# Optimization experiments

Hardware: AMD Instinct MI355X
Metric: run time of the kernel (lower is better)

## Reference

```python
import jax, jax.numpy as jnp
import numpy as np

N = 50000   # nodes
E = 640000  # edges
IN, H, OUT = 128, 128, 64
BN_EPS = 1e-5


def setup_inputs() -> dict:
    key = jax.random.key(0)
    ks = jax.random.split(key, 16)
    inp = {}
    inp["x"] = jax.random.normal(ks[0], (N, IN), jnp.float32)
    inp["edge_index"] = jax.random.randint(ks[1], (2, E), 0, N, dtype=jnp.int32)
    # BatchNorm affine params (nontrivial so grads are informative)
    inp["bn_in_gamma"] = 1.0 + 0.1 * jax.random.normal(ks[2], (IN,), jnp.float32)
    inp["bn_in_beta"] = 0.1 * jax.random.normal(ks[3], (IN,), jnp.float32)
    inp["bn1_gamma"] = 1.0 + 0.1 * jax.random.normal(ks[4], (H,), jnp.float32)
    inp["bn1_beta"] = 0.1 * jax.random.normal(ks[5], (H,), jnp.float32)
    inp["bn2_gamma"] = 1.0 + 0.1 * jax.random.normal(ks[6], (OUT,), jnp.float32)
    inp["bn2_beta"] = 0.1 * jax.random.normal(ks[7], (OUT,), jnp.float32)
    # Linear / GCNConv weights (fan-in scaled)
    inp["proj_W"] = jax.random.normal(ks[8], (IN, H), jnp.float32) / np.sqrt(IN)
    inp["proj_b"] = jnp.zeros((H,), jnp.float32)
    inp["conv1_W"] = jax.random.normal(ks[9], (H, H), jnp.float32) / np.sqrt(H)
    inp["conv1_b"] = jnp.zeros((H,), jnp.float32)
    inp["conv2_W"] = jax.random.normal(ks[10], (H, OUT), jnp.float32) / np.sqrt(H)
    inp["conv2_b"] = jnp.zeros((OUT,), jnp.float32)
    return inp


def batchnorm(x, gamma, beta):
    # training-mode BN: batch statistics (biased variance), per-feature affine
    m = jnp.mean(x, axis=0)
    v = jnp.mean(jnp.square(x - m), axis=0)
    return (x - m) * jax.lax.rsqrt(v + BN_EPS) * gamma + beta


def gcn_conv(x, src, dst, W, b):
    # PyG GCNConv: y = D^{-1/2} (A + I) D^{-1/2} (x W) + b
    xw = x @ W                                    # [N, F_out]
    loops = jnp.arange(N, dtype=src.dtype)
    s = jnp.concatenate([src, loops])             # [E + N]
    d = jnp.concatenate([dst, loops])
    deg = jax.ops.segment_sum(jnp.ones_like(d, jnp.float32), d, num_segments=N)
    dinv = jnp.where(deg > 0, jax.lax.rsqrt(deg), 0.0)
    norm = dinv[s] * dinv[d]                      # [E + N]
    msgs = xw[s] * norm[:, None]                  # gather + per-edge scale
    out = jax.ops.segment_sum(msgs, d, num_segments=N)  # scatter-add
    return out + b


def reference(x, edge_index, bn_in_gamma, bn_in_beta, bn1_gamma, bn1_beta,
              bn2_gamma, bn2_beta, proj_W, proj_b, conv1_W, conv1_b,
              conv2_W, conv2_b):
    src, dst = edge_index[0], edge_index[1]
    h = batchnorm(x, bn_in_gamma, bn_in_beta)
    h = jax.nn.relu(h @ proj_W + proj_b)
    h = jax.nn.relu(batchnorm(gcn_conv(h, src, dst, conv1_W, conv1_b),
                              bn1_gamma, bn1_beta))
    # dropout: identity in eval mode
    out = batchnorm(gcn_conv(h, src, dst, conv2_W, conv2_b),
                    bn2_gamma, bn2_beta)
    return out
```

## Files before the change

### kernel.cpp

```cpp
#include <hip/hip_runtime.h>

#define NN 50000
#define NE 640000
#define BNEPS 1e-5f
#define NBANK 16
#define CAP 64

#define OFF_DINV 0
#define OFF_CURSOR 51200
#define OFF_ESRC 102400
#define OFF_WT0 1702400
#define OFF_WT1 1710592
#define OFF_WT2 1718784
#define OFF_STATS 1726976
#define OFF_B0 1737216
#define OFF_B1 8137216

typedef __attribute__((ext_vector_type(8))) __bf16 bf16x8;
typedef __attribute__((ext_vector_type(4))) float f32x4;

__device__ __forceinline__ float uplo(unsigned int u) {
  unsigned int v = u << 16;
  return __builtin_bit_cast(float, v);
}
__device__ __forceinline__ float uphi(unsigned int u) {
  unsigned int v = u & 0xffff0000u;
  return __builtin_bit_cast(float, v);
}
__device__ __forceinline__ unsigned int f2bf(float f) {
  unsigned int u = __builtin_bit_cast(unsigned int, f);
  return (u + 0x7fffu + ((u >> 16) & 1u)) >> 16;
}

__global__ __launch_bounds__(256) void prep_k(
    const float* __restrict__ W0, const float* __restrict__ W1,
    const float* __restrict__ W2, unsigned short* __restrict__ T0,
    unsigned short* __restrict__ T1, unsigned short* __restrict__ T2,
    int* __restrict__ cursor, float* __restrict__ stats) {
  const int bid = blockIdx.x;
  const int tid = threadIdx.x;
  if (bid < 160) {
    int f = bid * 256 + tid;
    if (f < 16384) {
      int k = f >> 7, n = f & 127;
      T0[n * 128 + k] = (unsigned short)f2bf(W0[f]);
    } else if (f < 32768) {
      int g = f - 16384;
      int k = g >> 7, n = g & 127;
      T1[n * 128 + k] = (unsigned short)f2bf(W1[g]);
    } else if (f < 40960) {
      int g = f - 32768;
      int k = g >> 6, n = g & 63;
      T2[n * 128 + k] = (unsigned short)f2bf(W2[g]);
    }
  } else if (bid < 356) {
    int i = (bid - 160) * 256 + tid;
    if (i < NN) cursor[i] = i * CAP;
  } else {
    int j = (bid - 356) * 256 + tid;
    stats[j] = 0.0f;
  }
}

template <int NC, int MODE>
__device__ __forceinline__ void bn_stats_body(
    int sbid, int nsb, int tid, const float* __restrict__ A,
    const float* __restrict__ dinv, const float* __restrict__ cb,
    float* __restrict__ sums, float* __restrict__ sqs,
    float (*rs)[NC], float (*rq)[NC]) {
  constexpr int CG = NC / 4;
  constexpr int RG = 256 / CG;
  const int tc = tid % CG;
  const int tr = tid / CG;
  float cb0 = 0, cb1 = 0, cb2 = 0, cb3 = 0;
  if (MODE == 1) {
    cb0 = cb[tc * 4];
    cb1 = cb[tc * 4 + 1];
    cb2 = cb[tc * 4 + 2];
    cb3 = cb[tc * 4 + 3];
  }
  float s0 = 0, s1 = 0, s2 = 0, s3 = 0, q0 = 0, q1 = 0, q2 = 0, q3 = 0;
  const int stride = nsb * RG;
  for (int r = sbid * RG + tr; r < NN; r += stride) {
    float4 v = *(const float4*)&A[(size_t)r * NC + tc * 4];
    if (MODE == 1) {
      float di = dinv[r];
      v.x = fmaf(v.x, di, cb0);
      v.y = fmaf(v.y, di, cb1);
      v.z = fmaf(v.z, di, cb2);
      v.w = fmaf(v.w, di, cb3);
    }
    s0 += v.x; s1 += v.y; s2 += v.z; s3 += v.w;
    q0 += v.x * v.x; q1 += v.y * v.y; q2 += v.z * v.z; q3 += v.w * v.w;
  }
  rs[tr][tc * 4] = s0; rs[tr][tc * 4 + 1] = s1;
  rs[tr][tc * 4 + 2] = s2; rs[tr][tc * 4 + 3] = s3;
  rq[tr][tc * 4] = q0; rq[tr][tc * 4 + 1] = q1;
  rq[tr][tc * 4 + 2] = q2; rq[tr][tc * 4 + 3] = q3;
  __syncthreads();
  if (tr == 0) {
    const int bank = (sbid & (NBANK - 1)) * NC;
    for (int j = 0; j < 4; ++j) {
      int c = tc * 4 + j;
      float ts = 0, tq = 0;
      for (int g = 0; g < RG; ++g) { ts += rs[g][c]; tq += rq[g][c]; }
      atomicAdd(&sums[bank + c], ts);
      atomicAdd(&sqs[bank + c], tq);
    }
  }
}

template <int NC, int MODE>
__global__ __launch_bounds__(256) void bn_stats_k(const float* __restrict__ A,
                                                  const float* __restrict__ dinv,
                                                  const float* __restrict__ cb,
                                                  float* __restrict__ sums,
                                                  float* __restrict__ sqs) {
  __shared__ float rs[256 / (NC / 4)][NC];
  __shared__ float rq[256 / (NC / 4)][NC];
  bn_stats_body<NC, MODE>(blockIdx.x, gridDim.x, threadIdx.x, A, dinv, cb,
                          sums, sqs, rs, rq);
}

template <int NC, int PRE, int EPI>
__device__ __forceinline__ void gemm_body(
    int bid, int tid, char* __restrict__ smem, float* __restrict__ af_s,
    float* __restrict__ bf_s, const void* __restrict__ Ain,
    const unsigned short* __restrict__ Wt, const float* __restrict__ bias,
    const float* __restrict__ sums, const float* __restrict__ sqs,
    const float* __restrict__ gamma, const float* __restrict__ beta,
    const float* __restrict__ preb, const float* __restrict__ dinv,
    unsigned short* __restrict__ O1) {
  constexpr int TM = 64;
  constexpr int NTILES = NC / 16;
  constexpr int CSTR = NC + 4;
  const int row0 = bid * TM;

  if constexpr (PRE != 1) {
    if (tid < 128) {
      float s = 0.f, q = 0.f;
#pragma unroll
      for (int b = 0; b < NBANK; ++b) {
        s += sums[b * 128 + tid];
        q += sqs[b * 128 + tid];
      }
      float m = s * (1.0f / NN);
      float v = q * (1.0f / NN) - m * m;
      float a = gamma[tid] * rsqrtf(v + BNEPS);
      af_s[tid] = a;
      bf_s[tid] = beta[tid] - m * a;
    }
    __syncthreads();
    const float* A = (const float*)Ain;
    for (int f = tid; f < TM * 32; f += 256) {
      const int r = f >> 5;
      const int c4 = f & 31;
      const int rg = row0 + r;
      float4 v = make_float4(0.f, 0.f, 0.f, 0.f);
      if (rg < NN) {
        v = *(const float4*)&A[(size_t)rg * 128 + c4 * 4];
        const float4 a4 = *(const float4*)&af_s[c4 * 4];
        const float4 b4 = *(const float4*)&bf_s[c4 * 4];
        if (PRE == 0) {
          v.x = fmaf(a4.x, v.x, b4.x);
          v.y = fmaf(a4.y, v.y, b4.y);
          v.z = fmaf(a4.z, v.z, b4.z);
          v.w = fmaf(a4.w, v.w, b4.w);
        } else {
          const float di = dinv[rg];
          const float4 p4 = *(const float4*)&preb[c4 * 4];
          v.x = fmaxf(fmaf(a4.x, fmaf(di, v.x, p4.x), b4.x), 0.f);
          v.y = fmaxf(fmaf(a4.y, fmaf(di, v.y, p4.y), b4.y), 0.f);
          v.z = fmaxf(fmaf(a4.z, fmaf(di, v.z, p4.z), b4.z), 0.f);
          v.w = fmaxf(fmaf(a4.w, fmaf(di, v.w, p4.w), b4.w), 0.f);
        }
      }
      uint2 wv;
      wv.x = f2bf(v.x) | (f2bf(v.y) << 16);
      wv.y = f2bf(v.z) | (f2bf(v.w) << 16);
      const int ba = (r * 256 + c4 * 8) ^ ((r & 7) << 4);
      *(uint2*)(smem + ba) = wv;
    }
    __syncthreads();
  }

  const int w = tid >> 6;
  const int l = tid & 63;
  const int lr = l & 15;
  const int lg = l >> 4;
  f32x4 acc[NTILES];
#pragma unroll
  for (int i = 0; i < NTILES; ++i) acc[i] = (f32x4){0.f, 0.f, 0.f, 0.f};
  const int arow = w * 16 + lr;
#pragma unroll
  for (int kt = 0; kt < 4; ++kt) {
    bf16x8 a;
    if constexpr (PRE == 1) {
      const unsigned short* Ab = (const unsigned short*)Ain;
      a = __builtin_bit_cast(
          bf16x8,
          *(const uint4*)&Ab[(size_t)(row0 + arow) * 128 + kt * 32 + lg * 8]);
    } else {
      const int ba = (arow * 256 + kt * 64 + lg * 16) ^ ((arow & 7) << 4);
      a = __builtin_bit_cast(bf16x8, *(const uint4*)(smem + ba));
    }
#pragma unroll
    for (int nt = 0; nt < NTILES; ++nt) {
      bf16x8 b = __builtin_bit_cast(
          bf16x8,
          *(const uint4*)&Wt[(size_t)(nt * 16 + lr) * 128 + kt * 32 + lg * 8]);
      acc[nt] = __builtin_amdgcn_mfma_f32_16x16x32_bf16(a, b, acc[nt], 0, 0, 0);
    }
  }
  __syncthreads();

  float* Cl = (float*)smem;
#pragma unroll
  for (int nt = 0; nt < NTILES; ++nt)
#pragma unroll
    for (int r = 0; r < 4; ++r)
      Cl[(w * 16 + lg * 4 + r) * CSTR + nt * 16 + lr] = acc[nt][r];
  __syncthreads();

  constexpr int CG = NC / 4;
  constexpr int RPT = TM * CG / 256;
  const int tc = tid % CG;
  const int tr = tid / CG;
  float4 b4 = make_float4(0.f, 0.f, 0.f, 0.f);
  if constexpr (EPI == 0) b4 = *(const float4*)&bias[tc * 4];
#pragma unroll
  for (int i = 0; i < RPT; ++i) {
    const int row = tr * RPT + i;
    const int rg = row0 + row;
    if (rg < NN) {
      float4 v = *(const float4*)&Cl[row * CSTR + tc * 4];
      if (EPI == 0) {
        v.x = fmaxf(v.x + b4.x, 0.f);
        v.y = fmaxf(v.y + b4.y, 0.f);
        v.z = fmaxf(v.z + b4.z, 0.f);
        v.w = fmaxf(v.w + b4.w, 0.f);
      }
      uint2 o;
      o.x = f2bf(v.x) | (f2bf(v.y) << 16);
      o.y = f2bf(v.z) | (f2bf(v.w) << 16);
      *(uint2*)&O1[(size_t)rg * NC + tc * 4] = o;
    }
  }
}

__global__ __launch_bounds__(256) void gemm1_fill_k(
    const float* __restrict__ x, const unsigned short* __restrict__ Wt0,
    const float* __restrict__ proj_b, const float* __restrict__ s0,
    const float* __restrict__ q0, const float* __restrict__ g0,
    const float* __restrict__ b0, unsigned short* __restrict__ H1bf,
    const int* __restrict__ src, const int* __restrict__ dst,
    int* __restrict__ cursor, unsigned short* __restrict__ esrc) {
  __shared__ __align__(16) char smem[33792];
  __shared__ float af_s[128];
  __shared__ float bf_s[128];
  const int bid = blockIdx.x;
  const int tid = threadIdx.x;
  if (bid < 782) {
    gemm_body<128, 0, 0>(bid, tid, smem, af_s, bf_s, x, Wt0, proj_b, s0, q0,
                         g0, b0, nullptr, nullptr, H1bf);
  } else {
    int e = (bid - 782) * 256 + tid;
    if (e < NE) {
      int p = atomicAdd(&cursor[dst[e]], 1);
      esrc[p] = (unsigned short)src[e];
    }
  }
}

__global__ __launch_bounds__(256) void conv1_dinv_k(
    const unsigned short* __restrict__ H1bf,
    const unsigned short* __restrict__ Wt1, unsigned short* __restrict__ Ybf,
    const int* __restrict__ cursor, float* __restrict__ dinv) {
  __shared__ __align__(16) char smem[33792];
  __shared__ float af_s[128];
  __shared__ float bf_s[128];
  const int bid = blockIdx.x;
  const int tid = threadIdx.x;
  if (bid < 782) {
    gemm_body<128, 1, 2>(bid, tid, smem, af_s, bf_s, H1bf, Wt1, nullptr,
                         nullptr, nullptr, nullptr, nullptr, nullptr, nullptr,
                         Ybf);
  } else {
    int i = (bid - 782) * 256 + tid;
    if (i < NN) {
      int d = cursor[i] - i * CAP;
      dinv[i] = rsqrtf((float)d + 1.0f);
    }
  }
}

template <int NC>
__global__ __launch_bounds__(256) void gather_bf_k(
    const int* __restrict__ cursor, const unsigned short* __restrict__ esrc,
    const unsigned short* __restrict__ Y, const float* __restrict__ dinv,
    float* __restrict__ ACC) {
  constexpr int CG = NC / 8;
  constexpr int RG = 256 / CG;
  const int tc = threadIdx.x % CG;
  const int tr = threadIdx.x / CG;
  const int n = blockIdx.x * RG + tr;
  if (n >= NN) return;
  const int c = tc * 8;
  float a[8];
  {
    const float dn = dinv[n];
    const uint4 p = *(const uint4*)&Y[(size_t)n * NC + c];
    a[0] = dn * uplo(p.x); a[1] = dn * uphi(p.x);
    a[2] = dn * uplo(p.y); a[3] = dn * uphi(p.y);
    a[4] = dn * uplo(p.z); a[5] = dn * uphi(p.z);
    a[6] = dn * uplo(p.w); a[7] = dn * uphi(p.w);
  }
  const int beg = n * CAP;
  const int end = cursor[n];
  int e = beg;
  for (; e + 2 <= end; e += 2) {
    const int s0 = esrc[e];
    const int s1 = esrc[e + 1];
    const float d0 = dinv[s0];
    const float d1 = dinv[s1];
    const uint4 q0 = *(const uint4*)&Y[(size_t)s0 * NC + c];
    const uint4 q1 = *(const uint4*)&Y[(size_t)s1 * NC + c];
    a[0] = fmaf(d0, uplo(q0.x), a[0]); a[1] = fmaf(d0, uphi(q0.x), a[1]);
    a[2] = fmaf(d0, uplo(q0.y), a[2]); a[3] = fmaf(d0, uphi(q0.y), a[3]);
    a[4] = fmaf(d0, uplo(q0.z), a[4]); a[5] = fmaf(d0, uphi(q0.z), a[5]);
    a[6] = fmaf(d0, uplo(q0.w), a[6]); a[7] = fmaf(d0, uphi(q0.w), a[7]);
    a[0] = fmaf(d1, uplo(q1.x), a[0]); a[1] = fmaf(d1, uphi(q1.x), a[1]);
    a[2] = fmaf(d1, uplo(q1.y), a[2]); a[3] = fmaf(d1, uphi(q1.y), a[3]);
    a[4] = fmaf(d1, uplo(q1.z), a[4]); a[5] = fmaf(d1, uphi(q1.z), a[5]);
    a[6] = fmaf(d1, uplo(q1.w), a[6]); a[7] = fmaf(d1, uphi(q1.w), a[7]);
  }
  if (e < end) {
    const int s0 = esrc[e];
    const float d0 = dinv[s0];
    const uint4 q0 = *(const uint4*)&Y[(size_t)s0 * NC + c];
    a[0] = fmaf(d0, uplo(q0.x), a[0]); a[1] = fmaf(d0, uphi(q0.x), a[1]);
    a[2] = fmaf(d0, uplo(q0.y), a[2]); a[3] = fmaf(d0, uphi(q0.y), a[3]);
    a[4] = fmaf(d0, uplo(q0.z), a[4]); a[5] = fmaf(d0, uphi(q0.z), a[5]);
    a[6] = fmaf(d0, uplo(q0.w), a[6]); a[7] = fmaf(d0, uphi(q0.w), a[7]);
  }
  *(float4*)&ACC[(size_t)n * NC + c] = make_float4(a[0], a[1], a[2], a[3]);
  *(float4*)&ACC[(size_t)n * NC + c + 4] = make_float4(a[4], a[5], a[6], a[7]);
}

template <int NC, int PRE, int EPI>
__global__ __launch_bounds__(256) void mfma_gemm_k(
    const void* __restrict__ Ain, const unsigned short* __restrict__ Wt,
    const float* __restrict__ bias, const float* __restrict__ sums,
    const float* __restrict__ sqs, const float* __restrict__ gamma,
    const float* __restrict__ beta, const float* __restrict__ preb,
    const float* __restrict__ dinv, unsigned short* __restrict__ O1) {
  constexpr int CBYTES = 64 * (NC + 4) * 4;
  constexpr int SMEM = (CBYTES > 16384) ? CBYTES : 16384;
  __shared__ __align__(16) char smem[SMEM];
  __shared__ float af_s[128];
  __shared__ float bf_s[128];
  gemm_body<NC, PRE, EPI>(blockIdx.x, threadIdx.x, smem, af_s, bf_s, Ain, Wt,
                          bias, sums, sqs, gamma, beta, preb, dinv, O1);
}

__global__ __launch_bounds__(256) void final_k(
    const float* __restrict__ ACC2, const float* __restrict__ dinv,
    const float* __restrict__ cb, const float* __restrict__ s2,
    const float* __restrict__ q2, const float* __restrict__ gamma,
    const float* __restrict__ beta, float* __restrict__ out) {
  __shared__ float af_s[64];
  __shared__ float bf_s[64];
  if (threadIdx.x < 64) {
    float s = 0.f, q = 0.f;
#pragma unroll
    for (int b = 0; b < NBANK; ++b) {
      s += s2[b * 64 + threadIdx.x];
      q += q2[b * 64 + threadIdx.x];
    }
    float m = s * (1.0f / NN);
    float v = q * (1.0f / NN) - m * m;
    float a = gamma[threadIdx.x] * rsqrtf(v + BNEPS);
    af_s[threadIdx.x] = a;
    bf_s[threadIdx.x] = beta[threadIdx.x] - m * a;
  }
  __syncthreads();
  const int u = blockIdx.x * 256 + threadIdx.x;
  if (u >= NN * 16) return;
  const int r = u >> 4;
  const int c = (u & 15) * 4;
  const float di = dinv[r];
  float4 v = *(const float4*)&ACC2[(size_t)r * 64 + c];
  const float4 c4 = *(const float4*)&cb[c];
  const float4 a4 = *(const float4*)&af_s[c];
  const float4 b4 = *(const float4*)&bf_s[c];
  float4 o;
  o.x = fmaf(a4.x, fmaf(v.x, di, c4.x), b4.x);
  o.y = fmaf(a4.y, fmaf(v.y, di, c4.y), b4.y);
  o.z = fmaf(a4.z, fmaf(v.z, di, c4.z), b4.z);
  o.w = fmaf(a4.w, fmaf(v.w, di, c4.w), b4.w);
  *(float4*)&out[(size_t)r * 64 + c] = o;
}

extern "C" void kernel_launch(void* const* d_in, const int* in_sizes, int n_in,
                              void* d_out, int out_size, void* d_ws,
                              size_t ws_size, hipStream_t stream) {
  const float* x = (const float*)d_in[0];
  const int* ei = (const int*)d_in[1];
  const int* src = ei;
  const int* dst = ei + NE;
  const float* bn_in_g = (const float*)d_in[2];
  const float* bn_in_b = (const float*)d_in[3];
  const float* bn1_g = (const float*)d_in[4];
  const float* bn1_b = (const float*)d_in[5];
  const float* bn2_g = (const float*)d_in[6];
  const float* bn2_b = (const float*)d_in[7];
  const float* proj_W = (const float*)d_in[8];
  const float* proj_b = (const float*)d_in[9];
  const float* conv1_W = (const float*)d_in[10];
  const float* conv1_b = (const float*)d_in[11];
  const float* conv2_W = (const float*)d_in[12];
  const float* conv2_b = (const float*)d_in[13];
  float* out = (float*)d_out;

  float* ws = (float*)d_ws;
  float* dinv = ws + OFF_DINV;
  int* cursor = (int*)(ws + OFF_CURSOR);
  unsigned short* esrc = (unsigned short*)(ws + OFF_ESRC);
  unsigned short* Wt0 = (unsigned short*)(ws + OFF_WT0);
  unsigned short* Wt1 = (unsigned short*)(ws + OFF_WT1);
  unsigned short* Wt2 = (unsigned short*)(ws + OFF_WT2);
  float* st = ws + OFF_STATS;
  float* s0 = st;
  float* q0 = st + 2048;
  float* s1 = st + 4096;
  float* q1 = st + 6144;
  float* s2 = st + 8192;
  float* q2 = st + 9216;
  float* B0 = ws + OFF_B0;
  float* B1 = ws + OFF_B1;
  unsigned short* H1bf = (unsigned short*)B0;
  unsigned short* Ybf = (unsigned short*)B1;
  float* ACC = B0;
  unsigned short* Y2bf = (unsigned short*)B1;
  float* ACC2 = B0;

  prep_k<<<396, 256, 0, stream>>>(proj_W, conv1_W, conv2_W, Wt0, Wt1, Wt2,
                                  cursor, st);
  bn_stats_k<128, 0><<<1024, 256, 0, stream>>>(x, nullptr, nullptr, s0, q0);
  gemm1_fill_k<<<3282, 256, 0, stream>>>(x, Wt0, proj_b, s0, q0, bn_in_g,
                                         bn_in_b, H1bf, src, dst, cursor, esrc);
  conv1_dinv_k<<<978, 256, 0, stream>>>(H1bf, Wt1, Ybf, cursor, dinv);
  gather_bf_k<128><<<(NN + 15) / 16, 256, 0, stream>>>(cursor, esrc, Ybf, dinv,
                                                       ACC);
  bn_stats_k<128, 1><<<1024, 256, 0, stream>>>(ACC, dinv, conv1_b, s1, q1);
  mfma_gemm_k<64, 2, 2><<<782, 256, 0, stream>>>(
      ACC, Wt2, nullptr, s1, q1, bn1_g, bn1_b, conv1_b, dinv, Y2bf);
  gather_bf_k<64><<<(NN + 31) / 32, 256, 0, stream>>>(cursor, esrc, Y2bf, dinv,
                                                      ACC2);
  bn_stats_k<64, 1><<<1024, 256, 0, stream>>>(ACC2, dinv, conv2_b, s2, q2);
  final_k<<<(NN * 16 + 255) / 256, 256, 0, stream>>>(ACC2, dinv, conv2_b, s2,
                                                     q2, bn2_g, bn2_b, out);
}
```

Measured before the change: 177.8 us.

## Store conv1 aggregate as bf16 with folded bias and split edge fill across kernels

The first gather now applies the destination dinv scale and conv1 bias itself and writes a bf16 buffer instead of fp32. The BN1 stats pass and the second GEMM's prologue then read half the bytes, with a new bf16 stats kernel and a PRE==3 path in the GEMM. Separately, the CSR edge fill is split in half: one half rides along with the input BN stats kernel and the other with GEMM1, which removes a standalone stats launch's idle time. The trade-off is that BN1 statistics are computed from bf16-rounded values, which adds a small precision loss.

```diff
diff --git a/kernel.cpp b/kernel.cpp
--- a/kernel.cpp
+++ b/kernel.cpp
@@ -122,6 +122,40 @@
                           sums, sqs, rs, rq);
 }
 
+__global__ __launch_bounds__(256) void bn_stats_bf_k(
+    const unsigned short* __restrict__ Z, float* __restrict__ sums,
+    float* __restrict__ sqs) {
+  const int tc = threadIdx.x % 16;
+  const int tr = threadIdx.x / 16;
+  const int c = tc * 8;
+  float s[8], q[8];
+#pragma unroll
+  for (int j = 0; j < 8; ++j) { s[j] = 0.f; q[j] = 0.f; }
+  const int stride = gridDim.x * 16;
+  for (int r = blockIdx.x * 16 + tr; r < NN; r += stride) {
+    const uint4 p = *(const uint4*)&Z[(size_t)r * 128 + c];
+    float e[8] = {uplo(p.x), uphi(p.x), uplo(p.y), uphi(p.y),
+                  uplo(p.z), uphi(p.z), uplo(p.w), uphi(p.w)};
+#pragma unroll
+    for (int j = 0; j < 8; ++j) { s[j] += e[j]; q[j] += e[j] * e[j]; }
+  }
+  __shared__ float rs[16][128];
+  __shared__ float rq[16][128];
+#pragma unroll
+  for (int j = 0; j < 8; ++j) { rs[tr][c + j] = s[j]; rq[tr][c + j] = q[j]; }
+  __syncthreads();
+  if (tr == 0) {
+    const int bank = (blockIdx.x & (NBANK - 1)) * 128;
+#pragma unroll
+    for (int j = 0; j < 8; ++j) {
+      float ts = 0.f, tq = 0.f;
+      for (int g = 0; g < 16; ++g) { ts += rs[g][c + j]; tq += rq[g][c + j]; }
+      atomicAdd(&sums[bank + c + j], ts);
+      atomicAdd(&sqs[bank + c + j], tq);
+    }
+  }
+}
+
 template <int NC, int PRE, int EPI>
 __device__ __forceinline__ void gemm_body(
     int bid, int tid, char* __restrict__ smem, float* __restrict__ af_s,
@@ -129,7 +163,6 @@
     const unsigned short* __restrict__ Wt, const float* __restrict__ bias,
     const float* __restrict__ sums, const float* __restrict__ sqs,
     const float* __restrict__ gamma, const float* __restrict__ beta,
-    const float* __restrict__ preb, const float* __restrict__ dinv,
     unsigned short* __restrict__ O1) {
   constexpr int TM = 64;
   constexpr int NTILES = NC / 16;
@@ -151,35 +184,54 @@
       bf_s[tid] = beta[tid] - m * a;
     }
     __syncthreads();
-    const float* A = (const float*)Ain;
-    for (int f = tid; f < TM * 32; f += 256) {
-      const int r = f >> 5;
-      const int c4 = f & 31;
-      const int rg = row0 + r;
-      float4 v = make_float4(0.f, 0.f, 0.f, 0.f);
-      if (rg < NN) {
-        v = *(const float4*)&A[(size_t)rg * 128 + c4 * 4];
-        const float4 a4 = *(const float4*)&af_s[c4 * 4];
-        const float4 b4 = *(const float4*)&bf_s[c4 * 4];
-        if (PRE == 0) {
+    if constexpr (PRE == 0) {
+      const float* A = (const float*)Ain;
+      for (int f = tid; f < TM * 32; f += 256) {
+        const int r = f >> 5;
+        const int c4 = f & 31;
+        const int rg = row0 + r;
+        float4 v = make_float4(0.f, 0.f, 0.f, 0.f);
+        if (rg < NN) {
+          v = *(const float4*)&A[(size_t)rg * 128 + c4 * 4];
+          const float4 a4 = *(const float4*)&af_s[c4 * 4];
+          const float4 b4 = *(const float4*)&bf_s[c4 * 4];
           v.x = fmaf(a4.x, v.x, b4.x);
           v.y = fmaf(a4.y, v.y, b4.y);
           v.z = fmaf(a4.z, v.z, b4.z);
           v.w = fmaf(a4.w, v.w, b4.w);
-        } else {
-          const float di = dinv[rg];
-          const float4 p4 = *(const float4*)&preb[c4 * 4];
-          v.x = fmaxf(fmaf(a4.x, fmaf(di, v.x, p4.x), b4.x), 0.f);
-          v.y = fmaxf(fmaf(a4.y, fmaf(di, v.y, p4.y), b4.y), 0.f);
-          v.z = fmaxf(fmaf(a4.z, fmaf(di, v.z, p4.z), b4.z), 0.f);
-          v.w = fmaxf(fmaf(a4.w, fmaf(di, v.w, p4.w), b4.w), 0.f);
         }
+        uint2 wv;
+        wv.x = f2bf(v.x) | (f2bf(v.y) << 16);
+        wv.y = f2bf(v.z) | (f2bf(v.w) << 16);
+        const int ba = (r * 256 + c4 * 8) ^ ((r & 7) << 4);
+        *(uint2*)(smem + ba) = wv;
       }
-      uint2 wv;
-      wv.x = f2bf(v.x) | (f2bf(v.y) << 16);
-      wv.y = f2bf(v.z) | (f2bf(v.w) << 16);
-      const int ba = (r * 256 + c4 * 8) ^ ((r & 7) << 4);
-      *(uint2*)(smem + ba) = wv;
+    } else {
+      const unsigned short* Ab = (const unsigned short*)Ain;
+      for (int f = tid; f < TM * 16; f += 256) {
+        const int r = f >> 4;
+        const int c8 = f & 15;
+        const int rg = row0 + r;
+        uint4 w4 = make_uint4(0u, 0u, 0u, 0u);
+        if (rg < NN) {
+          const uint4 raw = *(const uint4*)&Ab[(size_t)rg * 128 + c8 * 8];
+          const int cc = c8 * 8;
+          float e[8] = {uplo(raw.x), uphi(raw.x), uplo(raw.y), uphi(raw.y),
+                        uplo(raw.z), uphi(raw.z), uplo(raw.w), uphi(raw.w)};
+          unsigned int p[4];
+#pragma unroll
+          for (int j = 0; j < 4; ++j) {
+            float lo = fmaxf(fmaf(af_s[cc + 2 * j], e[2 * j], bf_s[cc + 2 * j]), 0.f);
+            float hi = fmaxf(
+                fmaf(af_s[cc + 2 * j + 1], e[2 * j + 1], bf_s[cc + 2 * j + 1]),
+                0.f);
+            p[j] = f2bf(lo) | (f2bf(hi) << 16);
+          }
+          w4 = make_uint4(p[0], p[1], p[2], p[3]);
+        }
+        const int ba = (r * 256 + c8 * 16) ^ ((r & 7) << 4);
+        *(uint4*)(smem + ba) = w4;
+      }
     }
     __syncthreads();
   }
@@ -248,6 +300,26 @@
   }
 }
 
+__global__ __launch_bounds__(256) void stats_fill_k(
+    const float* __restrict__ x, float* __restrict__ s0,
+    float* __restrict__ q0, const int* __restrict__ src,
+    const int* __restrict__ dst, int* __restrict__ cursor,
+    unsigned short* __restrict__ esrc) {
+  __shared__ float rs[8][128];
+  __shared__ float rq[8][128];
+  const int bid = blockIdx.x;
+  if (bid < 1024) {
+    bn_stats_body<128, 0>(bid, 1024, threadIdx.x, x, nullptr, nullptr, s0, q0,
+                          rs, rq);
+  } else {
+    int e = (bid - 1024) * 256 + threadIdx.x;
+    if (e < NE / 2) {
+      int p = atomicAdd(&cursor[dst[e]], 1);
+      esrc[p] = (unsigned short)src[e];
+    }
+  }
+}
+
 __global__ __launch_bounds__(256) void gemm1_fill_k(
     const float* __restrict__ x, const unsigned short* __restrict__ Wt0,
     const float* __restrict__ proj_b, const float* __restrict__ s0,
@@ -262,9 +334,9 @@
   const int tid = threadIdx.x;
   if (bid < 782) {
     gemm_body<128, 0, 0>(bid, tid, smem, af_s, bf_s, x, Wt0, proj_b, s0, q0,
-                         g0, b0, nullptr, nullptr, H1bf);
+                         g0, b0, H1bf);
   } else {
-    int e = (bid - 782) * 256 + tid;
+    int e = NE / 2 + (bid - 782) * 256 + tid;
     if (e < NE) {
       int p = atomicAdd(&cursor[dst[e]], 1);
       esrc[p] = (unsigned short)src[e];
@@ -283,8 +355,7 @@
   const int tid = threadIdx.x;
   if (bid < 782) {
     gemm_body<128, 1, 2>(bid, tid, smem, af_s, bf_s, H1bf, Wt1, nullptr,
-                         nullptr, nullptr, nullptr, nullptr, nullptr, nullptr,
-                         Ybf);
+                         nullptr, nullptr, nullptr, nullptr, Ybf);
   } else {
     int i = (bid - 782) * 256 + tid;
     if (i < NN) {
@@ -294,11 +365,11 @@
   }
 }
 
-template <int NC>
+template <int NC, int OUTBF>
 __global__ __launch_bounds__(256) void gather_bf_k(
     const int* __restrict__ cursor, const unsigned short* __restrict__ esrc,
     const unsigned short* __restrict__ Y, const float* __restrict__ dinv,
-    float* __restrict__ ACC) {
+    void* __restrict__ outp, const float* __restrict__ cb) {
   constexpr int CG = NC / 8;
   constexpr int RG = 256 / CG;
   const int tc = threadIdx.x % CG;
@@ -306,9 +377,9 @@
   const int n = blockIdx.x * RG + tr;
   if (n >= NN) return;
   const int c = tc * 8;
+  const float dn = dinv[n];
   float a[8];
   {
-    const float dn = dinv[n];
     const uint4 p = *(const uint4*)&Y[(size_t)n * NC + c];
     a[0] = dn * uplo(p.x); a[1] = dn * uphi(p.x);
     a[2] = dn * uplo(p.y); a[3] = dn * uphi(p.y);
@@ -343,8 +414,22 @@
     a[4] = fmaf(d0, uplo(q0.z), a[4]); a[5] = fmaf(d0, uphi(q0.z), a[5]);
     a[6] = fmaf(d0, uplo(q0.w), a[6]); a[7] = fmaf(d0, uphi(q0.w), a[7]);
   }
-  *(float4*)&ACC[(size_t)n * NC + c] = make_float4(a[0], a[1], a[2], a[3]);
-  *(float4*)&ACC[(size_t)n * NC + c + 4] = make_float4(a[4], a[5], a[6], a[7]);
+  if constexpr (OUTBF == 1) {
+    unsigned int p[4];
+#pragma unroll
+    for (int j = 0; j < 4; ++j) {
+      float lo = fmaf(dn, a[2 * j], cb[c + 2 * j]);
+      float hi = fmaf(dn, a[2 * j + 1], cb[c + 2 * j + 1]);
+      p[j] = f2bf(lo) | (f2bf(hi) << 16);
+    }
+    *(uint4*)&((unsigned short*)outp)[(size_t)n * NC + c] =
+        make_uint4(p[0], p[1], p[2], p[3]);
+  } else {
+    float* ACC = (float*)outp;
+    *(float4*)&ACC[(size_t)n * NC + c] = make_float4(a[0], a[1], a[2], a[3]);
+    *(float4*)&ACC[(size_t)n * NC + c + 4] =
+        make_float4(a[4], a[5], a[6], a[7]);
+  }
 }
 
 template <int NC, int PRE, int EPI>
@@ -352,15 +437,14 @@
     const void* __restrict__ Ain, const unsigned short* __restrict__ Wt,
     const float* __restrict__ bias, const float* __restrict__ sums,
     const float* __restrict__ sqs, const float* __restrict__ gamma,
-    const float* __restrict__ beta, const float* __restrict__ preb,
-    const float* __restrict__ dinv, unsigned short* __restrict__ O1) {
+    const float* __restrict__ beta, unsigned short* __restrict__ O1) {
   constexpr int CBYTES = 64 * (NC + 4) * 4;
   constexpr int SMEM = (CBYTES > 16384) ? CBYTES : 16384;
   __shared__ __align__(16) char smem[SMEM];
   __shared__ float af_s[128];
   __shared__ float bf_s[128];
   gemm_body<NC, PRE, EPI>(blockIdx.x, threadIdx.x, smem, af_s, bf_s, Ain, Wt,
-                          bias, sums, sqs, gamma, beta, preb, dinv, O1);
+                          bias, sums, sqs, gamma, beta, O1);
 }
 
 __global__ __launch_bounds__(256) void final_k(
@@ -440,23 +524,23 @@
   float* B1 = ws + OFF_B1;
   unsigned short* H1bf = (unsigned short*)B0;
   unsigned short* Ybf = (unsigned short*)B1;
-  float* ACC = B0;
+  unsigned short* Z1bf = (unsigned short*)B0;
   unsigned short* Y2bf = (unsigned short*)B1;
   float* ACC2 = B0;
 
   prep_k<<<396, 256, 0, stream>>>(proj_W, conv1_W, conv2_W, Wt0, Wt1, Wt2,
                                   cursor, st);
-  bn_stats_k<128, 0><<<1024, 256, 0, stream>>>(x, nullptr, nullptr, s0, q0);
-  gemm1_fill_k<<<3282, 256, 0, stream>>>(x, Wt0, proj_b, s0, q0, bn_in_g,
+  stats_fill_k<<<2274, 256, 0, stream>>>(x, s0, q0, src, dst, cursor, esrc);
+  gemm1_fill_k<<<2032, 256, 0, stream>>>(x, Wt0, proj_b, s0, q0, bn_in_g,
                                          bn_in_b, H1bf, src, dst, cursor, esrc);
   conv1_dinv_k<<<978, 256, 0, stream>>>(H1bf, Wt1, Ybf, cursor, dinv);
-  gather_bf_k<128><<<(NN + 15) / 16, 256, 0, stream>>>(cursor, esrc, Ybf, dinv,
-                                                       ACC);
-  bn_stats_k<128, 1><<<1024, 256, 0, stream>>>(ACC, dinv, conv1_b, s1, q1);
-  mfma_gemm_k<64, 2, 2><<<782, 256, 0, stream>>>(
-      ACC, Wt2, nullptr, s1, q1, bn1_g, bn1_b, conv1_b, dinv, Y2bf);
-  gather_bf_k<64><<<(NN + 31) / 32, 256, 0, stream>>>(cursor, esrc, Y2bf, dinv,
-                                                      ACC2);
+  gather_bf_k<128, 1><<<(NN + 15) / 16, 256, 0, stream>>>(cursor, esrc, Ybf,
+                                                          dinv, Z1bf, conv1_b);
+  bn_stats_bf_k<<<1024, 256, 0, stream>>>(Z1bf, s1, q1);
+  mfma_gemm_k<64, 3, 2><<<782, 256, 0, stream>>>(Z1bf, Wt2, nullptr, s1, q1,
+                                                 bn1_g, bn1_b, Y2bf);
+  gather_bf_k<64, 0><<<(NN + 31) / 32, 256, 0, stream>>>(cursor, esrc, Y2bf,
+                                                         dinv, ACC2, nullptr);
   bn_stats_k<64, 1><<<1024, 256, 0, stream>>>(ACC2, dinv, conv2_b, s2, q2);
   final_k<<<(NN * 16 + 255) / 256, 256, 0, stream>>>(ACC2, dinv, conv2_b, s2,
                                                      q2, bn2_g, bn2_b, out);
```

Measured after the change: 176.1 us. No clear change (-0.9%).
